# Kernel tuning notes

Measured on AMD Instinct MI355X. Metric: run time of the kernel, lower is better.

## Reference

```python
import jax, jax.numpy as jnp
import numpy as np

N_ENT = 100000
N_REL = 237
IN_DIM = 128
OUT_DIM = 128
E = 400000


def setup_inputs() -> dict:
    key = jax.random.key(0)
    k1, k2, k3, k4, k5, k6, k7, k8 = jax.random.split(key, 8)
    src = jax.random.randint(k1, (E,), 0, N_ENT)
    dst = jax.random.randint(k2, (E,), 0, N_ENT)
    rel = jax.random.randint(k3, (E,), 0, N_REL)
    triplets = jnp.stack([src, dst, rel], axis=1)  # [E, 3]
    ent_embed = jax.random.normal(k4, (N_ENT, IN_DIM), dtype=jnp.float32)
    rel_embed = jax.random.normal(k5, (N_REL, IN_DIM), dtype=jnp.float32)
    # xavier_normal with gain=1.414 for weights; torch Linear bias ~ U(-1/sqrt(fan_in), 1/sqrt(fan_in))
    g = 1.414
    Wa = jax.random.normal(k6, (OUT_DIM, 3 * IN_DIM), dtype=jnp.float32) * (g * np.sqrt(2.0 / (3 * IN_DIM + OUT_DIM)))
    ba = jnp.zeros((OUT_DIM,), dtype=jnp.float32)
    Wa2 = jax.random.normal(k7, (1, OUT_DIM), dtype=jnp.float32) * (g * np.sqrt(2.0 / (OUT_DIM + 1)))
    ba2 = jnp.zeros((1,), dtype=jnp.float32)
    return {"triplets": triplets, "ent_embed": ent_embed, "rel_embed": rel_embed,
            "Wa": Wa, "ba": ba, "Wa2": Wa2, "ba2": ba2}


def reference(triplets, ent_embed, rel_embed, Wa, ba, Wa2, ba2):
    src, dst, rel = triplets[:, 0], triplets[:, 1], triplets[:, 2]
    # per-edge feature: [E, 3*in_dim]
    h = jnp.concatenate([ent_embed[src], rel_embed[rel], ent_embed[dst]], axis=1)
    c = h @ Wa.T + ba                                  # [E, out_dim]
    b = jax.nn.leaky_relu(c @ Wa2.T + ba2)             # [E, 1], slope 0.01
    e_b = jnp.exp(b)                                   # [E, 1]
    # segment-sum over source nodes (torch.sparse.sum over dim=1 of [N,N,F])
    e_b_sum = jax.ops.segment_sum(e_b, src, num_segments=N_ENT)       # [N, 1]
    temp1 = e_b * c                                    # [E, out_dim]
    h_sum = jax.ops.segment_sum(temp1, src, num_segments=N_ENT)       # [N, out_dim]
    ebs = jnp.where(e_b_sum == 0, 1e-12, e_b_sum)
    h_ent = h_sum / ebs                                # [N, out_dim]
    # scatter-mean of temp1 by relation id
    rel_sum = jax.ops.segment_sum(temp1, rel, num_segments=N_REL)     # [R, out_dim]
    rel_cnt = jax.ops.segment_sum(jnp.ones((temp1.shape[0], 1), temp1.dtype), rel, num_segments=N_REL)
    h_rel = rel_sum / jnp.maximum(rel_cnt, 1.0)        # [R, out_dim]
    return jax.nn.elu(h_ent), jax.nn.elu(h_rel)
```

## Files before the change

### kernel.cpp

```cpp
#include <hip/hip_runtime.h>
#include <math.h>

#define N_ENT 100000
#define N_REL 237
#define DIM   128
#define NE    400000


__global__ void k_transpose_wa(const float* __restrict__ Wa, float* __restrict__ WaT) {
    int i = blockIdx.x * 256 + threadIdx.x;
    if (i < 384 * 128) {
        int k = i >> 7, j = i & 127;
        WaT[i] = Wa[j * 384 + k];
    }
}

__global__ void k_proj_rel(const float* __restrict__ rel_e, const float* __restrict__ Wa,
                           const float* __restrict__ ba, float* __restrict__ Pr) {
    int i = blockIdx.x * 256 + threadIdx.x;
    if (i >= N_REL * DIM) return;
    int r = i >> 7, j = i & 127;
    float acc = ba[j];
    const float* wrow = Wa + j * 384 + 128;
    const float* erow = rel_e + r * DIM;
    #pragma unroll 8
    for (int k = 0; k < DIM; ++k) acc += erow[k] * wrow[k];
    Pr[i] = acc;
}

__global__ void k_qr(const float* __restrict__ Pr, const float* __restrict__ Wa2,
                     const float* __restrict__ ba2, float* __restrict__ qr) {
    const int lane = threadIdx.x & 63;
    const int r = (blockIdx.x * 256 + threadIdx.x) >> 6;
    if (r >= N_REL) return;
    float p = Pr[r * DIM + lane] * Wa2[lane] + Pr[r * DIM + 64 + lane] * Wa2[64 + lane];
    #pragma unroll
    for (int off = 32; off > 0; off >>= 1) p += __shfl_xor(p, off, 64);
    if (lane == 0) qr[r] = p + ba2[0];
}

#define KC 16
__global__ __launch_bounds__(256) void k_proj_ent(const float* __restrict__ ent,
        const float* __restrict__ WaT, const float* __restrict__ Wa2,
        float* __restrict__ Ps, float* __restrict__ Pd,
        float* __restrict__ qs, float* __restrict__ qd) {
    __shared__ float wsh[2 * KC * 132];
    const int tid = threadIdx.x;
    const int row0 = blockIdx.x * 64;
    const int rg = tid >> 4, cg = tid & 15;
    const int r0 = rg * 4, j0 = cg * 8;

    int rows[4];
    #pragma unroll
    for (int i = 0; i < 4; ++i) {
        int rr = row0 + r0 + i;
        rows[i] = (rr < N_ENT) ? rr : (N_ENT - 1);
    }

    float accs[4][8], accd[4][8];
    #pragma unroll
    for (int i = 0; i < 4; ++i)
        #pragma unroll
        for (int j = 0; j < 8; ++j) { accs[i][j] = 0.f; accd[i][j] = 0.f; }

    for (int kc = 0; kc < DIM; kc += KC) {
        if (kc) __syncthreads();
        for (int u = tid; u < 2 * KC * 32; u += 256) {
            int m   = u >> 9;
            int rem = u & 511;
            int kk  = rem >> 5, c4 = rem & 31;
            float4 v = *(const float4*)(WaT + (size_t)((m ? 256 : 0) + kc + kk) * 128 + c4 * 4);
            int perm = (c4 >> 1) + (c4 & 1) * 16;
            *(float4*)(wsh + m * KC * 132 + kk * 132 + perm * 4) = v;
        }
        __syncthreads();

        #pragma unroll
        for (int kq = 0; kq < 4; ++kq) {
            float ev[4][4];
            #pragma unroll
            for (int i = 0; i < 4; ++i) {
                float4 t = *(const float4*)(ent + (size_t)rows[i] * DIM + kc + kq * 4);
                ev[i][0] = t.x; ev[i][1] = t.y; ev[i][2] = t.z; ev[i][3] = t.w;
            }
            #pragma unroll
            for (int kk2 = 0; kk2 < 4; ++kk2) {
                int kk = kq * 4 + kk2;
                float4 a0 = *(float4*)(wsh + kk * 132 + cg * 4);
                float4 a1 = *(float4*)(wsh + kk * 132 + 64 + cg * 4);
                float4 b0 = *(float4*)(wsh + KC * 132 + kk * 132 + cg * 4);
                float4 b1 = *(float4*)(wsh + KC * 132 + kk * 132 + 64 + cg * 4);
                float ws[8] = {a0.x, a0.y, a0.z, a0.w, a1.x, a1.y, a1.z, a1.w};
                float wd[8] = {b0.x, b0.y, b0.z, b0.w, b1.x, b1.y, b1.z, b1.w};
                #pragma unroll
                for (int i = 0; i < 4; ++i) {
                    float e = ev[i][kk2];
                    #pragma unroll
                    for (int j = 0; j < 8; ++j) {
                        accs[i][j] += e * ws[j];
                        accd[i][j] += e * wd[j];
                    }
                }
            }
        }
    }

    #pragma unroll
    for (int i = 0; i < 4; ++i) {
        int row = row0 + r0 + i;
        if (row < N_ENT) {
            float4 o;
            o = make_float4(accs[i][0], accs[i][1], accs[i][2], accs[i][3]);
            *(float4*)(Ps + (size_t)row * DIM + j0) = o;
            o = make_float4(accs[i][4], accs[i][5], accs[i][6], accs[i][7]);
            *(float4*)(Ps + (size_t)row * DIM + j0 + 4) = o;
            o = make_float4(accd[i][0], accd[i][1], accd[i][2], accd[i][3]);
            *(float4*)(Pd + (size_t)row * DIM + j0) = o;
            o = make_float4(accd[i][4], accd[i][5], accd[i][6], accd[i][7]);
            *(float4*)(Pd + (size_t)row * DIM + j0 + 4) = o;
        }
    }

    __syncthreads();
    float4 w2a = *(const float4*)(Wa2 + j0);
    float4 w2b = *(const float4*)(Wa2 + j0 + 4);
    float w2v[8] = {w2a.x, w2a.y, w2a.z, w2a.w, w2b.x, w2b.y, w2b.z, w2b.w};
    #pragma unroll
    for (int i = 0; i < 4; ++i) {
        float p_s = 0.f, p_d = 0.f;
        #pragma unroll
        for (int j = 0; j < 8; ++j) { p_s += accs[i][j] * w2v[j]; p_d += accd[i][j] * w2v[j]; }
        wsh[(r0 + i) * 16 + cg]        = p_s;
        wsh[1024 + (r0 + i) * 16 + cg] = p_d;
    }
    __syncthreads();
    if (tid < 64) {
        int row = row0 + tid;
        if (row < N_ENT) {
            float ss = 0.f, sd = 0.f;
            #pragma unroll
            for (int c = 0; c < 16; ++c) {
                ss += wsh[tid * 16 + c];
                sd += wsh[1024 + tid * 16 + c];
            }
            qs[row] = ss;
            qd[row] = sd;
        }
    }
}

__global__ void k_hist2(const int* __restrict__ trip, int* __restrict__ scnt,
                        int* __restrict__ rcnt) {
    __shared__ int lh[N_REL];
    for (int i = threadIdx.x; i < N_REL; i += 256) lh[i] = 0;
    __syncthreads();
    int e0 = blockIdx.x * 1024 + threadIdx.x * 4;
    #pragma unroll
    for (int k = 0; k < 4; ++k) {
        int e = e0 + k;
        if (e < NE) {
            atomicAdd(scnt + trip[3 * e], 1);
            atomicAdd(&lh[trip[3 * e + 2]], 1);
        }
    }
    __syncthreads();
    for (int i = threadIdx.x; i < N_REL; i += 256)
        if (lh[i]) atomicAdd(rcnt + i, lh[i]);
}

__global__ void k_scan1(const int* __restrict__ cnt, int* __restrict__ escan,
                        int* __restrict__ bsum) {
    __shared__ int sh[256];
    const int t = threadIdx.x;
    int base = blockIdx.x * 1024 + t * 4;
    int v[4]; int s = 0;
    #pragma unroll
    for (int k = 0; k < 4; ++k) { int idx = base + k; v[k] = (idx < N_ENT) ? cnt[idx] : 0; s += v[k]; }
    sh[t] = s; __syncthreads();
    for (int off = 1; off < 256; off <<= 1) {
        int u = (t >= off) ? sh[t - off] : 0;
        __syncthreads();
        sh[t] += u;
        __syncthreads();
    }
    int run = sh[t] - s;
    #pragma unroll
    for (int k = 0; k < 4; ++k) { int idx = base + k; if (idx < N_ENT) escan[idx] = run; run += v[k]; }
    if (t == 255) bsum[blockIdx.x] = sh[255];
}

__global__ void k_scan2(int* __restrict__ bsum) {
    __shared__ int sh[128];
    const int t = threadIdx.x;
    int v = (t < 98) ? bsum[t] : 0;
    sh[t] = v; __syncthreads();
    for (int off = 1; off < 128; off <<= 1) {
        int u = (t >= off) ? sh[t - off] : 0;
        __syncthreads();
        sh[t] += u;
        __syncthreads();
    }
    if (t < 98) bsum[t] = sh[t] - v;
}

__global__ void k_scan3(int* __restrict__ row_start, const int* __restrict__ bsum,
                        int* __restrict__ cursor) {
    int i = blockIdx.x * 256 + threadIdx.x;
    if (i < N_ENT) {
        int v = row_start[i] + bsum[i >> 10];
        row_start[i] = v;
        cursor[i] = v;
    } else if (i == N_ENT) {
        row_start[N_ENT] = NE;
    }
}

__global__ void k_relscan(const int* __restrict__ rcnt, int* __restrict__ rrow,
                          int* __restrict__ rcursor) {
    __shared__ int sh[256];
    const int t = threadIdx.x;
    int v = (t < N_REL) ? rcnt[t] : 0;
    sh[t] = v; __syncthreads();
    for (int off = 1; off < 256; off <<= 1) {
        int u = (t >= off) ? sh[t - off] : 0;
        __syncthreads();
        sh[t] += u;
        __syncthreads();
    }
    int excl = sh[t] - v;
    if (t <= N_REL) rrow[t] = excl;
    if (t < N_REL) rcursor[t] = excl;
}

__global__ __launch_bounds__(256) void k_scatter3(const int* __restrict__ trip,
        int* __restrict__ scursor, int* __restrict__ rcursor,
        int2* __restrict__ sdr, int2* __restrict__ rsd) {
    __shared__ int lh[N_REL];
    __shared__ int lbase[N_REL];
    const int t = threadIdx.x;
    for (int i = t; i < N_REL; i += 256) lh[i] = 0;
    __syncthreads();

    const int e0 = blockIdx.x * 1024 + t * 4;
    int sv[4], dv[4], rv[4];
    #pragma unroll
    for (int k = 0; k < 4; ++k) {
        int e = e0 + k;
        if (e < NE) {
            sv[k] = trip[3 * e]; dv[k] = trip[3 * e + 1]; rv[k] = trip[3 * e + 2];
            atomicAdd(&lh[rv[k]], 1);
        } else { sv[k] = -1; }
    }
    __syncthreads();
    for (int i = t; i < N_REL; i += 256) {
        int c = lh[i];
        lbase[i] = c ? atomicAdd(rcursor + i, c) : 0;
        lh[i] = 0;
    }
    __syncthreads();
    #pragma unroll
    for (int k = 0; k < 4; ++k) {
        if (sv[k] >= 0) {
            int p1 = atomicAdd(scursor + sv[k], 1);
            sdr[p1] = make_int2(dv[k], rv[k]);
            int intra = atomicAdd(&lh[rv[k]], 1);
            rsd[lbase[rv[k]] + intra] = make_int2(sv[k], dv[k]);
        }
    }
}

__global__ __launch_bounds__(256) void k_seg(const int* __restrict__ row_start,
        const int2* __restrict__ sdr,
        const float* __restrict__ Ps, const float* __restrict__ Pd, const float* __restrict__ Pr,
        const float* __restrict__ qs, const float* __restrict__ qd, const float* __restrict__ qr,
        float* __restrict__ out) {
    const int lane = threadIdx.x & 63;
    const int s = (blockIdx.x * 256 + threadIdx.x) >> 6;
    if (s >= N_ENT) return;

    const int beg = row_start[s], end = row_start[s + 1];
    if (beg == end) {
        out[(size_t)s * DIM + lane] = 0.f;
        out[(size_t)s * DIM + 64 + lane] = 0.f;
        return;
    }
    const float myqs = qs[s];
    float acc0 = 0.f, acc1 = 0.f, ebs = 0.f;
    for (int j = beg; j < end; ++j) {
        int2 dr = sdr[j];
        float b = myqs + qr[dr.y] + qd[dr.x];
        b = (b > 0.f) ? b : 0.01f * b;
        float eb = expf(b);
        acc0 += eb * (Pr[dr.y * DIM + lane]      + Pd[(size_t)dr.x * DIM + lane]);
        acc1 += eb * (Pr[dr.y * DIM + 64 + lane] + Pd[(size_t)dr.x * DIM + 64 + lane]);
        ebs += eb;
    }
    float h0 = Ps[(size_t)s * DIM + lane]      + acc0 / ebs;
    float h1 = Ps[(size_t)s * DIM + 64 + lane] + acc1 / ebs;
    out[(size_t)s * DIM + lane]      = (h0 > 0.f) ? h0 : expm1f(h0);
    out[(size_t)s * DIM + 64 + lane] = (h1 > 0.f) ? h1 : expm1f(h1);
}

__global__ __launch_bounds__(1024) void k_relseg2(const int* __restrict__ rrow,
        const int2* __restrict__ rsd,
        const float* __restrict__ Ps, const float* __restrict__ Pd, const float* __restrict__ Pr,
        const float* __restrict__ qs, const float* __restrict__ qd, const float* __restrict__ qr,
        float* __restrict__ out) {
    __shared__ float red[16 * 128];
    __shared__ float reb[16];
    const int r = blockIdx.x;
    const int t = threadIdx.x;
    const int lane = t & 63;
    const int w = t >> 6;
    const float myqr = qr[r];

    const int beg = rrow[r], end = rrow[r + 1];
    float a0 = 0.f, a1 = 0.f, ebs = 0.f;
    for (int j = beg + w; j < end; j += 16) {
        int2 sd = rsd[j];
        float b = myqr + qs[sd.x] + qd[sd.y];
        b = (b > 0.f) ? b : 0.01f * b;
        float eb = expf(b);
        a0 += eb * (Ps[(size_t)sd.x * DIM + lane]      + Pd[(size_t)sd.y * DIM + lane]);
        a1 += eb * (Ps[(size_t)sd.x * DIM + 64 + lane] + Pd[(size_t)sd.y * DIM + 64 + lane]);
        ebs += eb;
    }
    red[w * 128 + lane]      = a0;
    red[w * 128 + 64 + lane] = a1;
    if (lane == 0) reb[w] = ebs;
    __syncthreads();
    if (t < 128) {
        float ssum = 0.f, et = 0.f;
        #pragma unroll
        for (int ww = 0; ww < 16; ++ww) { ssum += red[ww * 128 + t]; et += reb[ww]; }
        float h = (ssum + et * Pr[r * DIM + t]) / fmaxf((float)(end - beg), 1.0f);
        out[(size_t)N_ENT * DIM + r * DIM + t] = (h > 0.f) ? h : expm1f(h);
    }
}

extern "C" void kernel_launch(void* const* d_in, const int* in_sizes, int n_in,
                              void* d_out, int out_size, void* d_ws, size_t ws_size,
                              hipStream_t stream) {
    const int*   trip = (const int*)d_in[0];
    const float* ent  = (const float*)d_in[1];
    const float* rele = (const float*)d_in[2];
    const float* Wa   = (const float*)d_in[3];
    const float* ba   = (const float*)d_in[4];
    const float* Wa2  = (const float*)d_in[5];
    const float* ba2  = (const float*)d_in[6];
    float* out = (float*)d_out;

    float* ws  = (float*)d_ws;
    float* WaT = ws;
    float* Ps  = WaT + 384 * 128;
    float* Pd  = Ps + (size_t)N_ENT * DIM;
    float* Pr  = Pd + (size_t)N_ENT * DIM;
    float* qs  = Pr + N_REL * DIM;
    float* qd  = qs + N_ENT;
    float* qr  = qd + N_ENT;
    int* row_start = (int*)(qr + 240);
    int* cursor    = row_start + N_ENT + 1;
    int* rcnt      = cursor + N_ENT;
    int* rrow      = rcnt + 240;
    int* rcursor   = rrow + 240;
    int* bsum      = rcursor + 240;
    int2* sdr      = (int2*)(bsum + 128);
    int2* rsd      = sdr + NE;

    hipMemsetAsync(cursor, 0, (N_ENT + 240) * sizeof(int), stream);

    k_transpose_wa<<<192, 256, 0, stream>>>(Wa, WaT);
    k_proj_rel<<<(N_REL * DIM + 255) / 256, 256, 0, stream>>>(rele, Wa, ba, Pr);
    k_qr<<<(N_REL * 64 + 255) / 256, 256, 0, stream>>>(Pr, Wa2, ba2, qr);
    k_proj_ent<<<(N_ENT + 63) / 64, 256, 0, stream>>>(ent, WaT, Wa2, Ps, Pd, qs, qd);

    k_hist2<<<(NE + 1023) / 1024, 256, 0, stream>>>(trip, cursor, rcnt);
    k_scan1<<<98, 256, 0, stream>>>(cursor, row_start, bsum);
    k_scan2<<<1, 128, 0, stream>>>(bsum);
    k_scan3<<<(N_ENT + 256) / 256, 256, 0, stream>>>(row_start, bsum, cursor);
    k_relscan<<<1, 256, 0, stream>>>(rcnt, rrow, rcursor);
    k_scatter3<<<(NE + 1023) / 1024, 256, 0, stream>>>(trip, cursor, rcursor, sdr, rsd);

    k_seg<<<(N_ENT + 3) / 4, 256, 0, stream>>>(row_start, sdr, Ps, Pd, Pr,
                                               qs, qd, qr, out);
    k_relseg2<<<N_REL, 1024, 0, stream>>>(rrow, rsd, Ps, Pd, Pr, qs, qd, qr, out);
}
```

Measured before the change: 432.9 us.

## Use bf16 MFMA for entity projection and merge segment kernels into one launch

```diff
diff --git a/kernel.cpp b/kernel.cpp
--- a/kernel.cpp
+++ b/kernel.cpp
@@ -5,13 +5,35 @@
 #define N_REL 237
 #define DIM   128
 #define NE    400000
-
-
-__global__ void k_transpose_wa(const float* __restrict__ Wa, float* __restrict__ WaT) {
+#define SEGB  ((N_ENT + 15) / 16)
+
+typedef short bf16x8 __attribute__((ext_vector_type(8)));
+typedef float f32x4  __attribute__((ext_vector_type(4)));
+
+
+__device__ __forceinline__ unsigned short f2bf(float f) {
+    unsigned int u = __float_as_uint(f);
+    u += 0x7FFF + ((u >> 16) & 1);
+    return (unsigned short)(u >> 16);
+}
+
+__global__ void k_wah(const float* __restrict__ Wa, unsigned short* __restrict__ Wah) {
     int i = blockIdx.x * 256 + threadIdx.x;
-    if (i < 384 * 128) {
-        int k = i >> 7, j = i & 127;
-        WaT[i] = Wa[j * 384 + k];
+    if (i < 128 * 384) Wah[i] = f2bf(Wa[i]);
+}
+
+__global__ void k_vsd(const float* __restrict__ Wa, const float* __restrict__ Wa2,
+                      float* __restrict__ vs, float* __restrict__ vd) {
+    int t = threadIdx.x;
+    if (t < 128) {
+        float a = 0.f;
+        for (int j = 0; j < 128; ++j) a += Wa[j * 384 + t] * Wa2[j];
+        vs[t] = a;
+    } else if (t < 256) {
+        int k = t - 128;
+        float a = 0.f;
+        for (int j = 0; j < 128; ++j) a += Wa[j * 384 + 256 + k] * Wa2[j];
+        vd[k] = a;
     }
 }
 
@@ -39,113 +61,71 @@
     if (lane == 0) qr[r] = p + ba2[0];
 }
 
-#define KC 16
-__global__ __launch_bounds__(256) void k_proj_ent(const float* __restrict__ ent,
-        const float* __restrict__ WaT, const float* __restrict__ Wa2,
+__global__ __launch_bounds__(256) void k_proj_mfma(const float* __restrict__ ent,
+        const unsigned short* __restrict__ Wah,
+        const float* __restrict__ vs, const float* __restrict__ vd,
         float* __restrict__ Ps, float* __restrict__ Pd,
         float* __restrict__ qs, float* __restrict__ qd) {
-    __shared__ float wsh[2 * KC * 132];
-    const int tid = threadIdx.x;
-    const int row0 = blockIdx.x * 64;
-    const int rg = tid >> 4, cg = tid & 15;
-    const int r0 = rg * 4, j0 = cg * 8;
-
-    int rows[4];
-    #pragma unroll
-    for (int i = 0; i < 4; ++i) {
-        int rr = row0 + r0 + i;
-        rows[i] = (rr < N_ENT) ? rr : (N_ENT - 1);
-    }
-
-    float accs[4][8], accd[4][8];
-    #pragma unroll
-    for (int i = 0; i < 4; ++i)
+    const int wave = threadIdx.x >> 6, lane = threadIdx.x & 63;
+    const int row0 = blockIdx.x * 64 + wave * 16;
+    const int lr = lane & 15;
+    const int lg = lane >> 4;
+    const int arow = (row0 + lr < N_ENT) ? row0 + lr : (N_ENT - 1);
+
+    f32x4 accS[8], accD[8];
+    #pragma unroll
+    for (int t = 0; t < 8; ++t) {
+        accS[t] = (f32x4){0.f, 0.f, 0.f, 0.f};
+        accD[t] = (f32x4){0.f, 0.f, 0.f, 0.f};
+    }
+    float qsp = 0.f, qdp = 0.f;
+
+    #pragma unroll
+    for (int kk = 0; kk < 4; ++kk) {
+        const int k0 = kk * 32 + lg * 8;
+        const float* ep = ent + (size_t)arow * DIM + k0;
+        float4 e0 = *(const float4*)ep;
+        float4 e1 = *(const float4*)(ep + 4);
+        float4 v0 = *(const float4*)(vs + k0);
+        float4 v1 = *(const float4*)(vs + k0 + 4);
+        qsp += e0.x*v0.x + e0.y*v0.y + e0.z*v0.z + e0.w*v0.w
+             + e1.x*v1.x + e1.y*v1.y + e1.z*v1.z + e1.w*v1.w;
+        float4 u0 = *(const float4*)(vd + k0);
+        float4 u1 = *(const float4*)(vd + k0 + 4);
+        qdp += e0.x*u0.x + e0.y*u0.y + e0.z*u0.z + e0.w*u0.w
+             + e1.x*u1.x + e1.y*u1.y + e1.z*u1.z + e1.w*u1.w;
+        bf16x8 a;
+        a[0] = (short)f2bf(e0.x); a[1] = (short)f2bf(e0.y);
+        a[2] = (short)f2bf(e0.z); a[3] = (short)f2bf(e0.w);
+        a[4] = (short)f2bf(e1.x); a[5] = (short)f2bf(e1.y);
+        a[6] = (short)f2bf(e1.z); a[7] = (short)f2bf(e1.w);
         #pragma unroll
-        for (int j = 0; j < 8; ++j) { accs[i][j] = 0.f; accd[i][j] = 0.f; }
-
-    for (int kc = 0; kc < DIM; kc += KC) {
-        if (kc) __syncthreads();
-        for (int u = tid; u < 2 * KC * 32; u += 256) {
-            int m   = u >> 9;
-            int rem = u & 511;
-            int kk  = rem >> 5, c4 = rem & 31;
-            float4 v = *(const float4*)(WaT + (size_t)((m ? 256 : 0) + kc + kk) * 128 + c4 * 4);
-            int perm = (c4 >> 1) + (c4 & 1) * 16;
-            *(float4*)(wsh + m * KC * 132 + kk * 132 + perm * 4) = v;
-        }
-        __syncthreads();
-
-        #pragma unroll
-        for (int kq = 0; kq < 4; ++kq) {
-            float ev[4][4];
+        for (int t = 0; t < 8; ++t) {
+            const size_t wb = (size_t)(t * 16 + lr) * 384 + k0;
+            bf16x8 bs = *(const bf16x8*)(Wah + wb);
+            bf16x8 bd = *(const bf16x8*)(Wah + wb + 256);
+            accS[t] = __builtin_amdgcn_mfma_f32_16x16x32_bf16(a, bs, accS[t], 0, 0, 0);
+            accD[t] = __builtin_amdgcn_mfma_f32_16x16x32_bf16(a, bd, accD[t], 0, 0, 0);
+        }
+    }
+
+    #pragma unroll
+    for (int q = 0; q < 4; ++q) {
+        const int row = row0 + lg * 4 + q;
+        if (row < N_ENT) {
             #pragma unroll
-            for (int i = 0; i < 4; ++i) {
-                float4 t = *(const float4*)(ent + (size_t)rows[i] * DIM + kc + kq * 4);
-                ev[i][0] = t.x; ev[i][1] = t.y; ev[i][2] = t.z; ev[i][3] = t.w;
+            for (int t = 0; t < 8; ++t) {
+                Ps[(size_t)row * DIM + t * 16 + lr] = accS[t][q];
+                Pd[(size_t)row * DIM + t * 16 + lr] = accD[t][q];
             }
-            #pragma unroll
-            for (int kk2 = 0; kk2 < 4; ++kk2) {
-                int kk = kq * 4 + kk2;
-                float4 a0 = *(float4*)(wsh + kk * 132 + cg * 4);
-                float4 a1 = *(float4*)(wsh + kk * 132 + 64 + cg * 4);
-                float4 b0 = *(float4*)(wsh + KC * 132 + kk * 132 + cg * 4);
-                float4 b1 = *(float4*)(wsh + KC * 132 + kk * 132 + 64 + cg * 4);
-                float ws[8] = {a0.x, a0.y, a0.z, a0.w, a1.x, a1.y, a1.z, a1.w};
-                float wd[8] = {b0.x, b0.y, b0.z, b0.w, b1.x, b1.y, b1.z, b1.w};
-                #pragma unroll
-                for (int i = 0; i < 4; ++i) {
-                    float e = ev[i][kk2];
-                    #pragma unroll
-                    for (int j = 0; j < 8; ++j) {
-                        accs[i][j] += e * ws[j];
-                        accd[i][j] += e * wd[j];
-                    }
-                }
-            }
-        }
-    }
-
-    #pragma unroll
-    for (int i = 0; i < 4; ++i) {
-        int row = row0 + r0 + i;
-        if (row < N_ENT) {
-            float4 o;
-            o = make_float4(accs[i][0], accs[i][1], accs[i][2], accs[i][3]);
-            *(float4*)(Ps + (size_t)row * DIM + j0) = o;
-            o = make_float4(accs[i][4], accs[i][5], accs[i][6], accs[i][7]);
-            *(float4*)(Ps + (size_t)row * DIM + j0 + 4) = o;
-            o = make_float4(accd[i][0], accd[i][1], accd[i][2], accd[i][3]);
-            *(float4*)(Pd + (size_t)row * DIM + j0) = o;
-            o = make_float4(accd[i][4], accd[i][5], accd[i][6], accd[i][7]);
-            *(float4*)(Pd + (size_t)row * DIM + j0 + 4) = o;
-        }
-    }
-
-    __syncthreads();
-    float4 w2a = *(const float4*)(Wa2 + j0);
-    float4 w2b = *(const float4*)(Wa2 + j0 + 4);
-    float w2v[8] = {w2a.x, w2a.y, w2a.z, w2a.w, w2b.x, w2b.y, w2b.z, w2b.w};
-    #pragma unroll
-    for (int i = 0; i < 4; ++i) {
-        float p_s = 0.f, p_d = 0.f;
-        #pragma unroll
-        for (int j = 0; j < 8; ++j) { p_s += accs[i][j] * w2v[j]; p_d += accd[i][j] * w2v[j]; }
-        wsh[(r0 + i) * 16 + cg]        = p_s;
-        wsh[1024 + (r0 + i) * 16 + cg] = p_d;
-    }
-    __syncthreads();
-    if (tid < 64) {
-        int row = row0 + tid;
-        if (row < N_ENT) {
-            float ss = 0.f, sd = 0.f;
-            #pragma unroll
-            for (int c = 0; c < 16; ++c) {
-                ss += wsh[tid * 16 + c];
-                sd += wsh[1024 + tid * 16 + c];
-            }
-            qs[row] = ss;
-            qd[row] = sd;
-        }
+        }
+    }
+
+    qsp += __shfl_xor(qsp, 16, 64); qsp += __shfl_xor(qsp, 32, 64);
+    qdp += __shfl_xor(qdp, 16, 64); qdp += __shfl_xor(qdp, 32, 64);
+    if (lane < 16 && row0 + lane < N_ENT) {
+        qs[row0 + lane] = qsp;
+        qd[row0 + lane] = qdp;
     }
 }
 
@@ -269,72 +249,67 @@
     }
 }
 
-__global__ __launch_bounds__(256) void k_seg(const int* __restrict__ row_start,
-        const int2* __restrict__ sdr,
-        const float* __restrict__ Ps, const float* __restrict__ Pd, const float* __restrict__ Pr,
-        const float* __restrict__ qs, const float* __restrict__ qd, const float* __restrict__ qr,
-        float* __restrict__ out) {
-    const int lane = threadIdx.x & 63;
-    const int s = (blockIdx.x * 256 + threadIdx.x) >> 6;
-    if (s >= N_ENT) return;
-
-    const int beg = row_start[s], end = row_start[s + 1];
-    if (beg == end) {
-        out[(size_t)s * DIM + lane] = 0.f;
-        out[(size_t)s * DIM + 64 + lane] = 0.f;
-        return;
-    }
-    const float myqs = qs[s];
-    float acc0 = 0.f, acc1 = 0.f, ebs = 0.f;
-    for (int j = beg; j < end; ++j) {
-        int2 dr = sdr[j];
-        float b = myqs + qr[dr.y] + qd[dr.x];
-        b = (b > 0.f) ? b : 0.01f * b;
-        float eb = expf(b);
-        acc0 += eb * (Pr[dr.y * DIM + lane]      + Pd[(size_t)dr.x * DIM + lane]);
-        acc1 += eb * (Pr[dr.y * DIM + 64 + lane] + Pd[(size_t)dr.x * DIM + 64 + lane]);
-        ebs += eb;
-    }
-    float h0 = Ps[(size_t)s * DIM + lane]      + acc0 / ebs;
-    float h1 = Ps[(size_t)s * DIM + 64 + lane] + acc1 / ebs;
-    out[(size_t)s * DIM + lane]      = (h0 > 0.f) ? h0 : expm1f(h0);
-    out[(size_t)s * DIM + 64 + lane] = (h1 > 0.f) ? h1 : expm1f(h1);
-}
-
-__global__ __launch_bounds__(1024) void k_relseg2(const int* __restrict__ rrow,
+__global__ __launch_bounds__(1024) void k_edges(const int* __restrict__ rrow,
         const int2* __restrict__ rsd,
+        const int* __restrict__ row_start, const int2* __restrict__ sdr,
         const float* __restrict__ Ps, const float* __restrict__ Pd, const float* __restrict__ Pr,
         const float* __restrict__ qs, const float* __restrict__ qd, const float* __restrict__ qr,
         float* __restrict__ out) {
     __shared__ float red[16 * 128];
     __shared__ float reb[16];
-    const int r = blockIdx.x;
     const int t = threadIdx.x;
     const int lane = t & 63;
-    const int w = t >> 6;
-    const float myqr = qr[r];
-
-    const int beg = rrow[r], end = rrow[r + 1];
-    float a0 = 0.f, a1 = 0.f, ebs = 0.f;
-    for (int j = beg + w; j < end; j += 16) {
-        int2 sd = rsd[j];
-        float b = myqr + qs[sd.x] + qd[sd.y];
-        b = (b > 0.f) ? b : 0.01f * b;
-        float eb = expf(b);
-        a0 += eb * (Ps[(size_t)sd.x * DIM + lane]      + Pd[(size_t)sd.y * DIM + lane]);
-        a1 += eb * (Ps[(size_t)sd.x * DIM + 64 + lane] + Pd[(size_t)sd.y * DIM + 64 + lane]);
-        ebs += eb;
-    }
-    red[w * 128 + lane]      = a0;
-    red[w * 128 + 64 + lane] = a1;
-    if (lane == 0) reb[w] = ebs;
-    __syncthreads();
-    if (t < 128) {
-        float ssum = 0.f, et = 0.f;
-        #pragma unroll
-        for (int ww = 0; ww < 16; ++ww) { ssum += red[ww * 128 + t]; et += reb[ww]; }
-        float h = (ssum + et * Pr[r * DIM + t]) / fmaxf((float)(end - beg), 1.0f);
-        out[(size_t)N_ENT * DIM + r * DIM + t] = (h > 0.f) ? h : expm1f(h);
+
+    if (blockIdx.x < N_REL) {
+        const int r = blockIdx.x;
+        const int w = t >> 6;
+        const float myqr = qr[r];
+        const int beg = rrow[r], end = rrow[r + 1];
+        float a0 = 0.f, a1 = 0.f, ebs = 0.f;
+        for (int j = beg + w; j < end; j += 16) {
+            int2 sd = rsd[j];
+            float b = myqr + qs[sd.x] + qd[sd.y];
+            b = (b > 0.f) ? b : 0.01f * b;
+            float eb = expf(b);
+            a0 += eb * (Ps[(size_t)sd.x * DIM + lane]      + Pd[(size_t)sd.y * DIM + lane]);
+            a1 += eb * (Ps[(size_t)sd.x * DIM + 64 + lane] + Pd[(size_t)sd.y * DIM + 64 + lane]);
+            ebs += eb;
+        }
+        red[w * 128 + lane]      = a0;
+        red[w * 128 + 64 + lane] = a1;
+        if (lane == 0) reb[w] = ebs;
+        __syncthreads();
+        if (t < 128) {
+            float ssum = 0.f, et = 0.f;
+            #pragma unroll
+            for (int ww = 0; ww < 16; ++ww) { ssum += red[ww * 128 + t]; et += reb[ww]; }
+            float h = (ssum + et * Pr[r * DIM + t]) / fmaxf((float)(end - beg), 1.0f);
+            out[(size_t)N_ENT * DIM + r * DIM + t] = (h > 0.f) ? h : expm1f(h);
+        }
+    } else {
+        const int s = (blockIdx.x - N_REL) * 16 + (t >> 6);
+        if (s >= N_ENT) return;
+        const int beg = row_start[s], end = row_start[s + 1];
+        if (beg == end) {
+            out[(size_t)s * DIM + lane] = 0.f;
+            out[(size_t)s * DIM + 64 + lane] = 0.f;
+            return;
+        }
+        const float myqs = qs[s];
+        float acc0 = 0.f, acc1 = 0.f, ebs = 0.f;
+        for (int j = beg; j < end; ++j) {
+            int2 dr = sdr[j];
+            float b = myqs + qr[dr.y] + qd[dr.x];
+            b = (b > 0.f) ? b : 0.01f * b;
+            float eb = expf(b);
+            acc0 += eb * (Pr[dr.y * DIM + lane]      + Pd[(size_t)dr.x * DIM + lane]);
+            acc1 += eb * (Pr[dr.y * DIM + 64 + lane] + Pd[(size_t)dr.x * DIM + 64 + lane]);
+            ebs += eb;
+        }
+        float h0 = Ps[(size_t)s * DIM + lane]      + acc0 / ebs;
+        float h1 = Ps[(size_t)s * DIM + 64 + lane] + acc1 / ebs;
+        out[(size_t)s * DIM + lane]      = (h0 > 0.f) ? h0 : expm1f(h0);
+        out[(size_t)s * DIM + 64 + lane] = (h1 > 0.f) ? h1 : expm1f(h1);
     }
 }
 
@@ -351,14 +326,16 @@
     float* out = (float*)d_out;
 
     float* ws  = (float*)d_ws;
-    float* WaT = ws;
-    float* Ps  = WaT + 384 * 128;
+    float* Ps  = ws;
     float* Pd  = Ps + (size_t)N_ENT * DIM;
     float* Pr  = Pd + (size_t)N_ENT * DIM;
     float* qs  = Pr + N_REL * DIM;
     float* qd  = qs + N_ENT;
     float* qr  = qd + N_ENT;
-    int* row_start = (int*)(qr + 240);
+    float* vs  = qr + 240;
+    float* vd  = vs + 128;
+    unsigned short* Wah = (unsigned short*)(vd + 128);
+    int* row_start = (int*)(vd + 128 + 24576);
     int* cursor    = row_start + N_ENT + 1;
     int* rcnt      = cursor + N_ENT;
     int* rrow      = rcnt + 240;
@@ -369,10 +346,11 @@
 
     hipMemsetAsync(cursor, 0, (N_ENT + 240) * sizeof(int), stream);
 
-    k_transpose_wa<<<192, 256, 0, stream>>>(Wa, WaT);
+    k_wah<<<192, 256, 0, stream>>>(Wa, Wah);
+    k_vsd<<<1, 256, 0, stream>>>(Wa, Wa2, vs, vd);
     k_proj_rel<<<(N_REL * DIM + 255) / 256, 256, 0, stream>>>(rele, Wa, ba, Pr);
     k_qr<<<(N_REL * 64 + 255) / 256, 256, 0, stream>>>(Pr, Wa2, ba2, qr);
-    k_proj_ent<<<(N_ENT + 63) / 64, 256, 0, stream>>>(ent, WaT, Wa2, Ps, Pd, qs, qd);
+    k_proj_mfma<<<(N_ENT + 63) / 64, 256, 0, stream>>>(ent, Wah, vs, vd, Ps, Pd, qs, qd);
 
     k_hist2<<<(NE + 1023) / 1024, 256, 0, stream>>>(trip, cursor, rcnt);
     k_scan1<<<98, 256, 0, stream>>>(cursor, row_start, bsum);
@@ -381,7 +359,6 @@
     k_relscan<<<1, 256, 0, stream>>>(rcnt, rrow, rcursor);
     k_scatter3<<<(NE + 1023) / 1024, 256, 0, stream>>>(trip, cursor, rcursor, sdr, rsd);
 
-    k_seg<<<(N_ENT + 3) / 4, 256, 0, stream>>>(row_start, sdr, Ps, Pd, Pr,
-                                               qs, qd, qr, out);
-    k_relseg2<<<N_REL, 1024, 0, stream>>>(rrow, rsd, Ps, Pd, Pr, qs, qd, qr, out);
-}
+    k_edges<<<N_REL + SEGB, 1024, 0, stream>>>(rrow, rsd, row_start, sdr,
+                                               Ps, Pd, Pr, qs, qd, qr, out);
+}
```

After: 389.6 us. -10.0%, faster.
